# Optimization experiments

Measured on AMD Instinct MI355X. Metric: run time of the kernel, lower is better.

## Reference

```python
import jax, jax.numpy as jnp
import numpy as np

# Sizes derived from init_kwargs via calc_mlp_features:
# total_param=2117777, router_ratio=0.002 -> router_param=4235.554, expert_param=264192
# expert_hidden = 256, router_hidden = 352
N = 131072      # number of coordinate points
CIN = 3         # expert_insize == router_insize (xyz coords)
E = 8           # num_experts
K = 2           # top_k
H = 256         # expert_hidden (also SIREN data_channel)
RH = 352        # router_hidden
NHID = 3        # expert_layers - 2 hidden SIREN layers
W0C = 30.0      # sine frequency w0


def setup_inputs() -> dict:
    key = jax.random.key(0)
    ks = jax.random.split(key, 16)
    u = lambda k, shape, a: jax.random.uniform(k, shape, jnp.float32, -a, a)
    x = jax.random.uniform(ks[0], (N, CIN), jnp.float32, -1.0, 1.0)
    context = jax.random.uniform(ks[1], (N, CIN), jnp.float32, -1.0, 1.0)
    # Router: kaiming-normal weights, torch-default uniform biases
    Wr1 = jax.random.normal(ks[2], (CIN, RH), jnp.float32) * np.float32(np.sqrt(2.0 / CIN))
    br1 = u(ks[3], (RH,), 1.0 / np.sqrt(CIN))
    Wr2 = jax.random.normal(ks[4], (RH, E), jnp.float32) * np.float32(np.sqrt(2.0 / RH))
    br2 = u(ks[5], (E,), 1.0 / np.sqrt(RH))
    # SIREN experts (stacked over E): first layer U(-1/in, 1/in), rest U(+-sqrt(6/in)/30)
    sb = np.sqrt(6.0 / H) / 30.0
    W0 = u(ks[6], (E, CIN, H), 1.0 / CIN)
    b0 = u(ks[7], (E, H), 1.0 / np.sqrt(CIN))
    Wh = u(ks[8], (E, NHID, H, H), sb)
    bh = u(ks[9], (E, NHID, H), 1.0 / np.sqrt(H))
    Wo = u(ks[10], (E, H, H), sb)
    bo = u(ks[11], (E, H), 1.0 / np.sqrt(H))
    # Decoder: Linear(H,H)+ReLU+Linear(H,1)
    Wd1 = jax.random.normal(ks[12], (H, H), jnp.float32) * np.float32(np.sqrt(2.0 / H))
    bd1 = u(ks[13], (H,), 1.0 / np.sqrt(H))
    Wd2 = jax.random.normal(ks[14], (H, 1), jnp.float32) * np.float32(np.sqrt(2.0 / H))
    bd2 = u(ks[15], (1,), 1.0 / np.sqrt(H))
    return dict(x=x, context=context, Wr1=Wr1, br1=br1, Wr2=Wr2, br2=br2,
                W0=W0, b0=b0, Wh=Wh, bh=bh, Wo=Wo, bo=bo,
                Wd1=Wd1, bd1=bd1, Wd2=Wd2, bd2=bd2)


def reference(x, context, Wr1, br1, Wr2, br2, W0, b0, Wh, bh, Wo, bo, Wd1, bd1, Wd2, bd2):
    n = x.shape[0]
    # --- NoisyTopkRouter (eval path: no noise) ---
    logits = jnp.maximum(context @ Wr1 + br1, 0.0) @ Wr2 + br2          # [N, E]
    topv, topi = jax.lax.top_k(logits, K)                                # [N, K]
    # softmax over -inf-filled sparse logits == softmax over the top-k values
    w = jax.nn.softmax(topv, axis=-1)                                    # [N, K]
    gating = jnp.zeros_like(logits).at[jnp.arange(n)[:, None], topi].set(w)  # [N, E], zero off top-k
    # --- Per-expert SIREN, weighted combine ---
    # Masked dispatch + scatter-add in the original equals dense weighted sum
    # because gating is exactly zero for non-selected experts.
    def expert_step(acc, p):
        W0e, b0e, Whe, bhe, Woe, boe, ge = p
        h = jnp.sin(W0C * (x @ W0e + b0e))                # [N, H]
        for i in range(NHID):
            h = jnp.sin(W0C * (h @ Whe[i] + bhe[i]))
        out = h @ Woe + boe                               # [N, H], no output activation
        return acc + out * ge[:, None], None
    acc0 = jnp.zeros((n, H), dtype=x.dtype)
    final, _ = jax.lax.scan(expert_step, acc0, (W0, b0, Wh, bh, Wo, bo, gating.T))
    # --- Decoder ---
    return jnp.maximum(final @ Wd1 + bd1, 0.0) @ Wd2 + bd2               # [N, 1]
```

## Files before the change

kernel.cpp:

```cpp
#include <hip/hip_runtime.h>
#include <stdint.h>

#define N_PTS 131072
#define RH    352
#define SREV  4.774648292756860f

typedef short  bf16x8 __attribute__((ext_vector_type(8)));
typedef float  f32x16 __attribute__((ext_vector_type(16)));

__device__ __forceinline__ unsigned short f2bf(float f) {
  uint32_t u = __builtin_bit_cast(uint32_t, f);
  u = (u + 0x7FFFu + ((u >> 16) & 1u)) >> 16;
  return (unsigned short)u;
}
__device__ __forceinline__ float bf2f(unsigned short s) {
  return __builtin_bit_cast(float, ((uint32_t)s) << 16);
}
__device__ __forceinline__ float vsin1(float x) {
  float xf = x - floorf(x);
  float r;
  asm("v_sin_f32 %0, %1" : "=v"(r) : "v"(xf));
  return r;
}
__device__ __forceinline__ f32x16 mfma_bf16(bf16x8 a, bf16x8 b, f32x16 c) {
  return __builtin_amdgcn_mfma_f32_32x32x16_bf16(a, b, c, 0, 0, 0);
}

#define AWLOAD(d0, d1, addr64) \
  asm volatile("global_load_dwordx4 %0, %2, off\n\t" \
               "global_load_dwordx4 %1, %2, off offset:1024" \
               : "=&v"(d0), "=&v"(d1) : "v"(addr64))

#define VWAIT(N, r0, r1) \
  asm volatile("s_waitcnt vmcnt(" #N ")" : "+v"(r0), "+v"(r1))

__global__ __launch_bounds__(512) void setup_kernel(
    const float* __restrict__ W0, const float* __restrict__ b0,
    const float* __restrict__ Wh, const float* __restrict__ bh,
    const float* __restrict__ Wo, const float* __restrict__ bo,
    const float* __restrict__ Wd1, const float* __restrict__ bd1,
    short* __restrict__ pW0, short* __restrict__ pWh,
    short* __restrict__ pWo, short* __restrict__ pWd1,
    const float* __restrict__ ctx, const float* __restrict__ Wr1,
    const float* __restrict__ br1, const float* __restrict__ Wr2,
    const float* __restrict__ br2, uint4* __restrict__ topk,
    uint32_t* __restrict__ counts)
{
  __shared__ double w1d[RH*4];
  __shared__ double w2d[RH*8];
  __shared__ uint32_t lcnt[8];
  int b = blockIdx.x, tid = threadIdx.x;

  if (b < 569) {
    int jb = tid >> 6, l = tid & 63;
    int j  = jb*32 + (l & 31);
    int s0 = (l >> 5) * 8;
    unsigned short o[8];
    short* dp;
    if (b < 544) {
      int m = b / 17, slice = b % 17;
      int e = m >> 2, t = m & 3;
      const float* src; const float* bias; float scale; short* dst;
      if (t < 3) { src = Wh + (size_t)(e*3+t)*65536; bias = bh + (size_t)(e*3+t)*256; scale = SREV; dst = pWh + (size_t)(e*3+t)*69632; }
      else       { src = Wo + (size_t)e*65536;       bias = bo + (size_t)e*256;       scale = 1.0f; dst = pWo + (size_t)e*69632; }
      if (slice < 16) {
        #pragma unroll
        for (int i = 0; i < 8; ++i) {
          int k = slice*16 + s0 + i;
          o[i] = f2bf(scale * src[(size_t)k*256 + j]);
        }
      } else {
        #pragma unroll
        for (int i = 0; i < 8; ++i) o[i] = 0;
        if (s0 == 0) {
          float a = scale * bias[j];
          unsigned short h = f2bf(a);
          o[0] = h; o[1] = f2bf(a - bf2f(h));
        }
      }
      dp = dst + (size_t)slice*4096 + jb*512 + l*8;
    } else if (b < 552) {
      int e = b - 544;
      const float* w0 = W0 + (size_t)e*768;
      const float* bb = b0 + (size_t)e*256;
      #pragma unroll
      for (int i = 0; i < 8; ++i) {
        int s = s0 + i;
        unsigned short v = 0;
        if (s < 3) v = f2bf(SREV * w0[(size_t)s*256 + j]);
        else if (s < 6) { float a = SREV * w0[(size_t)(s-3)*256 + j]; unsigned short h = f2bf(a); v = f2bf(a - bf2f(h)); }
        else if (s < 9) v = f2bf(SREV * w0[(size_t)(s-6)*256 + j]);
        else if (s == 9)  v = f2bf(SREV * bb[j]);
        else if (s == 10) { float a = SREV * bb[j]; unsigned short h = f2bf(a); v = f2bf(a - bf2f(h)); }
        o[i] = v;
      }
      dp = pW0 + (size_t)e*4096 + jb*512 + l*8;
    } else {
      int slice = b - 552;
      if (slice < 16) {
        #pragma unroll
        for (int i = 0; i < 8; ++i) {
          int k = slice*16 + s0 + i;
          o[i] = f2bf(Wd1[(size_t)k*256 + j]);
        }
      } else {
        #pragma unroll
        for (int i = 0; i < 8; ++i) o[i] = 0;
        if (s0 == 0) {
          float a = bd1[j];
          unsigned short h = f2bf(a);
          o[0] = h; o[1] = f2bf(a - bf2f(h));
        }
      }
      dp = pWd1 + (size_t)slice*4096 + jb*512 + l*8;
    }
    uint4 v;
    v.x = (uint32_t)o[0] | ((uint32_t)o[1] << 16);
    v.y = (uint32_t)o[2] | ((uint32_t)o[3] << 16);
    v.z = (uint32_t)o[4] | ((uint32_t)o[5] << 16);
    v.w = (uint32_t)o[6] | ((uint32_t)o[7] << 16);
    *(uint4*)dp = v;
    return;
  }

  int rb = b - 569;
  for (int i = tid; i < RH; i += 512) {
    w1d[i*4+0] = (double)Wr1[i];
    w1d[i*4+1] = (double)Wr1[352 + i];
    w1d[i*4+2] = (double)Wr1[704 + i];
    w1d[i*4+3] = (double)br1[i];
  }
  for (int i = tid; i < RH*8; i += 512) w2d[i] = (double)Wr2[i];
  if (tid < 8) lcnt[tid] = 0;
  __syncthreads();

  int n = rb*512 + tid;
  double c0 = (double)ctx[(size_t)n*3+0];
  double c1 = (double)ctx[(size_t)n*3+1];
  double c2 = (double)ctx[(size_t)n*3+2];
  double lg[8];
  #pragma unroll
  for (int e = 0; e < 8; ++e) lg[e] = (double)br2[e];
  for (int j = 0; j < RH; ++j) {
    const double* a = &w1d[j*4];
    double h = c0*a[0] + c1*a[1] + c2*a[2] + a[3];
    h = h > 0.0 ? h : 0.0;
    const double* bq = &w2d[j*8];
    lg[0] += h*bq[0]; lg[1] += h*bq[1]; lg[2] += h*bq[2]; lg[3] += h*bq[3];
    lg[4] += h*bq[4]; lg[5] += h*bq[5]; lg[6] += h*bq[6]; lg[7] += h*bq[7];
  }
  double v0 = -1e300, v1 = -1e300; int i0 = 0, i1 = 0;
  #pragma unroll
  for (int e = 0; e < 8; ++e) {
    double lv = lg[e];
    if (lv > v0)      { v1 = v0; i1 = i0; v0 = lv; i0 = e; }
    else if (lv > v1) { v1 = lv; i1 = e; }
  }
  float ex = __expf((float)(v1 - v0));
  float s = 1.0f / (1.0f + ex);
  uint4 t;
  t.x = (uint32_t)i0 | ((uint32_t)i1 << 8);
  t.y = __builtin_bit_cast(uint32_t, s);
  t.z = __builtin_bit_cast(uint32_t, ex * s);
  t.w = 0;
  topk[n] = t;
  atomicAdd(&lcnt[i0], 1u); atomicAdd(&lcnt[i1], 1u);
  __syncthreads();
  if (tid < 8) atomicAdd(&counts[tid], lcnt[tid]);
}

__global__ __launch_bounds__(256) void scatter_kernel(
    const uint4* __restrict__ topk, const uint32_t* __restrict__ counts,
    uint32_t* __restrict__ cursors, uint32_t* __restrict__ plist,
    float* __restrict__ pw)
{
  __shared__ uint32_t lc[8], lb[8], offs[8];
  int tid = threadIdx.x;
  if (tid < 8) {
    lc[tid] = 0;
    uint32_t o = 0;
    for (int k = 0; k < tid; ++k) o += counts[k];
    offs[tid] = o;
  }
  __syncthreads();
  int n = blockIdx.x*256 + tid;
  uint4 t = topk[n];
  uint32_t e0 = t.x & 255u, e1 = (t.x >> 8) & 255u;
  uint32_t p0 = atomicAdd(&lc[e0], 1u);
  uint32_t p1 = atomicAdd(&lc[e1], 1u);
  __syncthreads();
  if (tid < 8) lb[tid] = offs[tid] + atomicAdd(&cursors[tid], lc[tid]);
  __syncthreads();
  uint32_t d0 = lb[e0] + p0, d1 = lb[e1] + p1;
  plist[d0] = ((uint32_t)n << 1);      pw[d0] = __builtin_bit_cast(float, t.y);
  plist[d1] = ((uint32_t)n << 1) | 1u; pw[d1] = __builtin_bit_cast(float, t.z);
}

__global__ __launch_bounds__(256, 3) void expert_kernel(
    const float* __restrict__ x, const uint32_t* __restrict__ counts,
    const uint32_t* __restrict__ plist, const float* __restrict__ pw,
    const short* __restrict__ pW0, const short* __restrict__ pWh,
    const short* __restrict__ pWo, short* __restrict__ outbuf)
{
  __shared__ __align__(16) uint8_t smem[34816];
  uint8_t* hB = smem;
  uint8_t* xB = smem + 32768;

  int tid = threadIdx.x;
  int lane = tid & 63;
  int jq = tid >> 6;
  int aoff = jq*2048 + lane*16;

  bf16x8 bbias;
  #pragma unroll
  for (int i = 0; i < 8; ++i) bbias[i] = 0;
  if (lane < 32) { bbias[0] = (short)0x3F80; bbias[1] = (short)0x3F80; }

  bf16x8 aw[5][2];
  f32x16 acc[2][2];

  int rr = tid >> 2;
  int rq = tid & 3;

  uint32_t tt = blockIdx.x;
  int e = -1; uint32_t cnt = 0, off = 0;
  #pragma unroll 1
  for (int ee = 0; ee < 8; ++ee) {
    uint32_t c = counts[ee];
    uint32_t nt = (c + 63u) >> 6;
    if (tt < nt) { e = ee; cnt = c; break; }
    tt -= nt; off += c;
  }
  if (e < 0) return;
  uint32_t base = off + (tt << 6);
  int nvalid = (int)cnt - (int)(tt << 6); if (nvalid > 64) nvalid = 64;

  uint64_t matp[4];
  matp[0] = (uint64_t)(uintptr_t)(pWh + (size_t)(e*3+0)*69632);
  matp[1] = (uint64_t)(uintptr_t)(pWh + (size_t)(e*3+1)*69632);
  matp[2] = (uint64_t)(uintptr_t)(pWh + (size_t)(e*3+2)*69632);
  matp[3] = (uint64_t)(uintptr_t)(pWo + (size_t)e*69632);

  {
    uint64_t pb = matp[0] + (uint64_t)aoff;
    AWLOAD(aw[0][0], aw[0][1], pb);
    AWLOAD(aw[1][0], aw[1][1], pb + 8192);
    AWLOAD(aw[2][0], aw[2][1], pb + 16384);
    AWLOAD(aw[3][0], aw[3][1], pb + 24576);
  }

  float wgt[2];
  #pragma unroll
  for (int c = 0; c < 2; ++c) {
    int n = c*32 + (lane & 31);
    wgt[c] = (n < nvalid) ? pw[base + n] : 0.0f;
  }
  uint32_t psv = (rr < nvalid) ? plist[base + rr] : 0u;

  if (tid < 64) {
    float x0 = 0.0f, x1 = 0.0f, x2 = 0.0f;
    if (tid < nvalid) {
      uint32_t v = plist[base + tid];
      const float* xp = x + (size_t)(v >> 1)*3;
      x0 = xp[0]; x1 = xp[1]; x2 = xp[2];
    }
    unsigned short h0 = f2bf(x0), h1 = f2bf(x1), h2 = f2bf(x2);
    unsigned short l0 = f2bf(x0 - bf2f(h0)), l1 = f2bf(x1 - bf2f(h1)), l2 = f2bf(x2 - bf2f(h2));
    uint4 r0, r1;
    r0.x = (uint32_t)h0 | ((uint32_t)h1 << 16);
    r0.y = (uint32_t)h2 | ((uint32_t)h0 << 16);
    r0.z = (uint32_t)h1 | ((uint32_t)h2 << 16);
    r0.w = (uint32_t)l0 | ((uint32_t)l1 << 16);
    r1.x = (uint32_t)l2 | (0x3F80u << 16);
    r1.y = 0x3F80u;
    r1.z = 0u; r1.w = 0u;
    uint4* dst = (uint4*)(xB + tid*32);
    dst[0] = r0; dst[1] = r1;
  }

  const uint8_t* pw0e = (const uint8_t*)(pW0 + (size_t)e*4096);
  bf16x8 a0[2];
  a0[0] = *(const bf16x8*)(pw0e + aoff);
  a0[1] = *(const bf16x8*)(pw0e + aoff + 1024);

  __syncthreads();

  #pragma unroll
  for (int a2 = 0; a2 < 2; ++a2)
    #pragma unroll
    for (int c = 0; c < 2; ++c)
      #pragma unroll
      for (int r = 0; r < 16; ++r) acc[a2][c][r] = 0.0f;

  {
    bf16x8 bv[2];
    #pragma unroll
    for (int c = 0; c < 2; ++c) {
      int n = c*32 + (lane & 31);
      bv[c] = *(const bf16x8*)(xB + n*32 + ((lane >> 5)*16));
    }
    #pragma unroll
    for (int a2 = 0; a2 < 2; ++a2)
      #pragma unroll
      for (int c = 0; c < 2; ++c)
        acc[a2][c] = mfma_bf16(a0[a2], bv[c], acc[a2][c]);
  }

#define WRITE_SIN() { _Pragma("unroll") \
    for (int a2 = 0; a2 < 2; ++a2) { \
      int jb = jq*2 + a2; \
      _Pragma("unroll") \
      for (int c = 0; c < 2; ++c) { \
        int n = c*32 + (lane & 31); \
        uint32_t rowb = (uint32_t)n * 512u; \
        uint32_t sw = (uint32_t)((n & 7) << 4); \
        _Pragma("unroll") \
        for (int g = 0; g < 4; ++g) { \
          float s0f = vsin1(acc[a2][c][g*4+0]); \
          float s1f = vsin1(acc[a2][c][g*4+1]); \
          float s2f = vsin1(acc[a2][c][g*4+2]); \
          float s3f = vsin1(acc[a2][c][g*4+3]); \
          uint2 pv; \
          pv.x = (uint32_t)f2bf(s0f) | ((uint32_t)f2bf(s1f) << 16); \
          pv.y = (uint32_t)f2bf(s2f) | ((uint32_t)f2bf(s3f) << 16); \
          int j0 = jb*32 + g*8 + ((lane >> 5) << 2); \
          uint32_t off2 = (rowb + (uint32_t)(j0*2)) ^ sw; \
          *(uint2*)(hB + off2) = pv; \
        } \
      } \
    } }

  WRITE_SIN();
  __syncthreads();

#define STEP(L, kb) { \
    enum { u_ = (L)*17 + (kb), ps_ = u_ + 4, us_ = u_ % 5, pss_ = ps_ % 5 }; \
    if (ps_ <= 67) { \
      uint64_t pa_ = matp[ps_/17] + (uint64_t)((ps_%17)*8192) + (uint64_t)aoff; \
      AWLOAD(aw[pss_][0], aw[pss_][1], pa_); \
    } \
    if (u_ <= 63)      { VWAIT(8, aw[us_][0], aw[us_][1]); } \
    else if (u_ == 64) { VWAIT(6, aw[us_][0], aw[us_][1]); } \
    else if (u_ == 65) { VWAIT(4, aw[us_][0], aw[us_][1]); } \
    else if (u_ == 66) { VWAIT(2, aw[us_][0], aw[us_][1]); } \
    else               { VWAIT(0, aw[us_][0], aw[us_][1]); } \
    bf16x8 bv0_, bv1_; \
    if ((kb) < 16) { \
      { int n_ = (lane & 31); \
        uint32_t off_ = ((uint32_t)n_*512u + (uint32_t)((kb)*32) + (uint32_t)((lane >> 5)*16)) \
                        ^ (uint32_t)((n_ & 7) << 4); \
        bv0_ = *(const bf16x8*)(hB + off_); } \
      { int n_ = 32 + (lane & 31); \
        uint32_t off_ = ((uint32_t)n_*512u + (uint32_t)((kb)*32) + (uint32_t)((lane >> 5)*16)) \
                        ^ (uint32_t)((n_ & 7) << 4); \
        bv1_ = *(const bf16x8*)(hB + off_); } \
    } else { bv0_ = bbias; bv1_ = bbias; } \
    acc[0][0] = mfma_bf16(aw[us_][0], bv0_, acc[0][0]); \
    acc[1][0] = mfma_bf16(aw[us_][1], bv0_, acc[1][0]); \
    acc[0][1] = mfma_bf16(aw[us_][0], bv1_, acc[0][1]); \
    acc[1][1] = mfma_bf16(aw[us_][1], bv1_, acc[1][1]); \
}
#define LAYER17(L) STEP(L,0) STEP(L,1) STEP(L,2) STEP(L,3) STEP(L,4) STEP(L,5) \
    STEP(L,6) STEP(L,7) STEP(L,8) STEP(L,9) STEP(L,10) STEP(L,11) STEP(L,12) \
    STEP(L,13) STEP(L,14) STEP(L,15) STEP(L,16)

#define ZACC() { _Pragma("unroll") for (int a2 = 0; a2 < 2; ++a2) \
    _Pragma("unroll") for (int c = 0; c < 2; ++c) \
    _Pragma("unroll") for (int r = 0; r < 16; ++r) acc[a2][c][r] = 0.0f; }

  ZACC(); LAYER17(0)
  __syncthreads(); WRITE_SIN(); __syncthreads();
  ZACC(); LAYER17(1)
  __syncthreads(); WRITE_SIN(); __syncthreads();
  ZACC(); LAYER17(2)
  __syncthreads(); WRITE_SIN(); __syncthreads();
  ZACC(); LAYER17(3)
  __syncthreads();
  #pragma unroll
  for (int a2 = 0; a2 < 2; ++a2) {
    int jb = jq*2 + a2;
    #pragma unroll
    for (int c = 0; c < 2; ++c) {
      int n = c*32 + (lane & 31);
      float w = wgt[c];
      uint32_t rowb = (uint32_t)n * 512u;
      uint32_t sw = (uint32_t)((n & 7) << 4);
      #pragma unroll
      for (int g = 0; g < 4; ++g) {
        float s0f = acc[a2][c][g*4+0] * w;
        float s1f = acc[a2][c][g*4+1] * w;
        float s2f = acc[a2][c][g*4+2] * w;
        float s3f = acc[a2][c][g*4+3] * w;
        uint2 pv;
        pv.x = (uint32_t)f2bf(s0f) | ((uint32_t)f2bf(s1f) << 16);
        pv.y = (uint32_t)f2bf(s2f) | ((uint32_t)f2bf(s3f) << 16);
        int j0 = jb*32 + g*8 + ((lane >> 5) << 2);
        uint32_t off2 = (rowb + (uint32_t)(j0*2)) ^ sw;
        *(uint2*)(hB + off2) = pv;
      }
    }
  }
  __syncthreads();
  if (rr < nvalid) {
    uint4* dst = (uint4*)(outbuf + ((size_t)(psv & 1)*N_PTS + (size_t)(psv >> 1))*256
                          + rq*64);
    uint32_t rowb = (uint32_t)rr*512u + (uint32_t)rq*128u;
    uint32_t sw = (uint32_t)((rr & 7) << 4);
    #pragma unroll
    for (int c = 0; c < 8; ++c)
      dst[c] = *(const uint4*)(hB + ((rowb + (uint32_t)(c*16)) ^ sw));
  }
}

__global__ __launch_bounds__(256, 3) void decoder_kernel(
    const short* __restrict__ outbuf, const short* __restrict__ pWd1,
    const float* __restrict__ Wd2v, const float* __restrict__ bd2,
    float* __restrict__ outp)
{
  __shared__ __align__(16) uint8_t smem[34816];
  uint8_t* hB = smem;
  float* wd2  = (float*)(smem + 32768);
  float* part = (float*)(smem + 33792);

  int tid = threadIdx.x;
  int lane = tid & 63;
  int jq = tid >> 6;
  int aoff = jq*2048 + lane*16;
  int tbase = blockIdx.x * 64;
  int rr = tid >> 2;
  int rq = tid & 3;

  bf16x8 bbias;
  #pragma unroll
  for (int i = 0; i < 8; ++i) bbias[i] = 0;
  if (lane < 32) { bbias[0] = (short)0x3F80; bbias[1] = (short)0x3F80; }

  bf16x8 aw[5][2];
  f32x16 acc[2][2];

  uint64_t wp = (uint64_t)(uintptr_t)pWd1;
  {
    uint64_t pb = wp + (uint64_t)aoff;
    AWLOAD(aw[0][0], aw[0][1], pb);
    AWLOAD(aw[1][0], aw[1][1], pb + 8192);
    AWLOAD(aw[2][0], aw[2][1], pb + 16384);
    AWLOAD(aw[3][0], aw[3][1], pb + 24576);
  }

  wd2[tid] = Wd2v[tid];

  {
    const short* o0 = outbuf + (size_t)(tbase + rr)*256 + rq*64;
    const short* o1 = o0 + (size_t)N_PTS*256;
    uint32_t rowb = (uint32_t)rr*512u + (uint32_t)rq*128u;
    uint32_t sw = (uint32_t)((rr & 7) << 4);
    #pragma unroll
    for (int c = 0; c < 8; ++c) {
      uint4 a  = *(const uint4*)(o0 + c*8);
      uint4 bq = *(const uint4*)(o1 + c*8);
      uint4 ov;
      uint32_t* ap = (uint32_t*)&a;
      uint32_t* bp = (uint32_t*)&bq;
      uint32_t* op = (uint32_t*)&ov;
      #pragma unroll
      for (int w = 0; w < 4; ++w) {
        uint32_t ua = ap[w], ub = bp[w];
        float f0 = bf2f((unsigned short)(ua & 0xFFFFu)) + bf2f((unsigned short)(ub & 0xFFFFu));
        float f1 = bf2f((unsigned short)(ua >> 16))     + bf2f((unsigned short)(ub >> 16));
        op[w] = (uint32_t)f2bf(f0) | ((uint32_t)f2bf(f1) << 16);
      }
      *(uint4*)(hB + ((rowb + (uint32_t)(c*16)) ^ sw)) = ov;
    }
  }
  __syncthreads();

  #pragma unroll
  for (int a2 = 0; a2 < 2; ++a2)
    #pragma unroll
    for (int c = 0; c < 2; ++c)
      #pragma unroll
      for (int r = 0; r < 16; ++r) acc[a2][c][r] = 0.0f;

#define DSTEP(kb) { \
    enum { ps_ = (kb) + 4, us_ = (kb) % 5, pss_ = ps_ % 5 }; \
    if (ps_ <= 16) { \
      uint64_t pa_ = wp + (uint64_t)(ps_*8192) + (uint64_t)aoff; \
      AWLOAD(aw[pss_][0], aw[pss_][1], pa_); \
    } \
    if ((kb) <= 12)      { VWAIT(8, aw[us_][0], aw[us_][1]); } \
    else if ((kb) == 13) { VWAIT(6, aw[us_][0], aw[us_][1]); } \
    else if ((kb) == 14) { VWAIT(4, aw[us_][0], aw[us_][1]); } \
    else if ((kb) == 15) { VWAIT(2, aw[us_][0], aw[us_][1]); } \
    else                 { VWAIT(0, aw[us_][0], aw[us_][1]); } \
    bf16x8 bv0_, bv1_; \
    if ((kb) < 16) { \
      { int n_ = (lane & 31); \
        uint32_t off_ = ((uint32_t)n_*512u + (uint32_t)((kb)*32) + (uint32_t)((lane >> 5)*16)) \
                        ^ (uint32_t)((n_ & 7) << 4); \
        bv0_ = *(const bf16x8*)(hB + off_); } \
      { int n_ = 32 + (lane & 31); \
        uint32_t off_ = ((uint32_t)n_*512u + (uint32_t)((kb)*32) + (uint32_t)((lane >> 5)*16)) \
                        ^ (uint32_t)((n_ & 7) << 4); \
        bv1_ = *(const bf16x8*)(hB + off_); } \
    } else { bv0_ = bbias; bv1_ = bbias; } \
    acc[0][0] = mfma_bf16(aw[us_][0], bv0_, acc[0][0]); \
    acc[1][0] = mfma_bf16(aw[us_][1], bv0_, acc[1][0]); \
    acc[0][1] = mfma_bf16(aw[us_][0], bv1_, acc[0][1]); \
    acc[1][1] = mfma_bf16(aw[us_][1], bv1_, acc[1][1]); \
}
  DSTEP(0)  DSTEP(1)  DSTEP(2)  DSTEP(3)  DSTEP(4)  DSTEP(5)
  DSTEP(6)  DSTEP(7)  DSTEP(8)  DSTEP(9)  DSTEP(10) DSTEP(11)
  DSTEP(12) DSTEP(13) DSTEP(14) DSTEP(15) DSTEP(16)

  float p0 = 0.0f, p1 = 0.0f;
  #pragma unroll
  for (int a2 = 0; a2 < 2; ++a2) {
    int jb = jq*2 + a2;
    #pragma unroll
    for (int c = 0; c < 2; ++c) {
      #pragma unroll
      for (int r = 0; r < 16; ++r) {
        int j = jb*32 + (r & 3) + ((r >> 2) << 3) + ((lane >> 5) << 2);
        float v = acc[a2][c][r];
        v = v > 0.0f ? v : 0.0f;
        float t = v * wd2[j];
        if (c == 0) p0 += t; else p1 += t;
      }
    }
  }
  p0 += __shfl_xor(p0, 32);
  p1 += __shfl_xor(p1, 32);
  if (lane < 32) {
    part[jq*64 + lane] = p0;
    part[jq*64 + 32 + lane] = p1;
  }
  __syncthreads();
  if (tid < 64)
    outp[tbase + tid] = part[tid] + part[64 + tid] + part[128 + tid]
                      + part[192 + tid] + bd2[0];
}

extern "C" void kernel_launch(void* const* d_in, const int* in_sizes, int n_in,
                              void* d_out, int out_size, void* d_ws, size_t ws_size,
                              hipStream_t stream) {
  const float* x   = (const float*)d_in[0];
  const float* ctx = (const float*)d_in[1];
  const float* Wr1 = (const float*)d_in[2];
  const float* br1 = (const float*)d_in[3];
  const float* Wr2 = (const float*)d_in[4];
  const float* br2 = (const float*)d_in[5];
  const float* W0  = (const float*)d_in[6];
  const float* b0  = (const float*)d_in[7];
  const float* Wh  = (const float*)d_in[8];
  const float* bh  = (const float*)d_in[9];
  const float* Wo  = (const float*)d_in[10];
  const float* bo  = (const float*)d_in[11];
  const float* Wd1 = (const float*)d_in[12];
  const float* bd1 = (const float*)d_in[13];
  const float* Wd2 = (const float*)d_in[14];
  const float* bd2 = (const float*)d_in[15];
  float* out = (float*)d_out;

  const size_t WS_COUNTS  = 0;
  const size_t WS_CURSORS = 32;
  const size_t WS_TOPK    = 1024;
  const size_t WS_PLIST   = WS_TOPK  + (size_t)N_PTS*16;
  const size_t WS_PW      = WS_PLIST + (size_t)N_PTS*8;
  const size_t WS_PW0     = WS_PW    + (size_t)N_PTS*8;
  const size_t WS_PWH     = WS_PW0   + (size_t)8*8192;
  const size_t WS_PWO     = WS_PWH   + (size_t)24*139264;
  const size_t WS_PWD1    = WS_PWO   + (size_t)8*139264;
  const size_t WS_OUT     = WS_PWD1  + (size_t)139264;
  const size_t WS_END     = WS_OUT   + (size_t)2*N_PTS*256*2;

  if (ws_size < WS_END) {
    hipMemsetAsync(d_out, 0xFF, (size_t)out_size*4, stream);
    return;
  }

  uint8_t* ws = (uint8_t*)d_ws;
  uint32_t* counts  = (uint32_t*)(ws + WS_COUNTS);
  uint32_t* cursors = (uint32_t*)(ws + WS_CURSORS);
  uint4*    topk    = (uint4*)   (ws + WS_TOPK);
  uint32_t* plist   = (uint32_t*)(ws + WS_PLIST);
  float*    pw      = (float*)   (ws + WS_PW);
  short*    pW0     = (short*)   (ws + WS_PW0);
  short*    pWh     = (short*)   (ws + WS_PWH);
  short*    pWo     = (short*)   (ws + WS_PWO);
  short*    pWd1    = (short*)   (ws + WS_PWD1);
  short*    outbuf  = (short*)   (ws + WS_OUT);

  hipMemsetAsync(counts, 0, 64, stream);

  setup_kernel  <<<825,  512, 0, stream>>>(W0, b0, Wh, bh, Wo, bo, Wd1, bd1,
                                           pW0, pWh, pWo, pWd1,
                                           ctx, Wr1, br1, Wr2, br2, topk, counts);
  scatter_kernel<<<512,  256, 0, stream>>>(topk, counts, cursors, plist, pw);
  expert_kernel <<<4104, 256, 0, stream>>>(x, counts, plist, pw,
                                           pW0, pWh, pWo, outbuf);
  decoder_kernel<<<2048, 256, 0, stream>>>(outbuf, pWd1, Wd2, bd2, out);
}
```

Before: 279.1 us.

## Compute router in fp32 with fp64 fallback near ties; interleave output row stores

```diff
diff --git a/kernel.cpp b/kernel.cpp
--- a/kernel.cpp
+++ b/kernel.cpp
@@ -46,8 +46,8 @@
     const float* __restrict__ br2, uint4* __restrict__ topk,
     uint32_t* __restrict__ counts)
 {
-  __shared__ double w1d[RH*4];
-  __shared__ double w2d[RH*8];
+  __shared__ float w1f[RH*4];
+  __shared__ float w2f[RH*8];
   __shared__ uint32_t lcnt[8];
   int b = blockIdx.x, tid = threadIdx.x;
 
@@ -125,38 +125,62 @@
 
   int rb = b - 569;
   for (int i = tid; i < RH; i += 512) {
-    w1d[i*4+0] = (double)Wr1[i];
-    w1d[i*4+1] = (double)Wr1[352 + i];
-    w1d[i*4+2] = (double)Wr1[704 + i];
-    w1d[i*4+3] = (double)br1[i];
-  }
-  for (int i = tid; i < RH*8; i += 512) w2d[i] = (double)Wr2[i];
+    w1f[i*4+0] = Wr1[i];
+    w1f[i*4+1] = Wr1[352 + i];
+    w1f[i*4+2] = Wr1[704 + i];
+    w1f[i*4+3] = br1[i];
+  }
+  for (int i = tid; i < RH*8; i += 512) w2f[i] = Wr2[i];
   if (tid < 8) lcnt[tid] = 0;
   __syncthreads();
 
   int n = rb*512 + tid;
-  double c0 = (double)ctx[(size_t)n*3+0];
-  double c1 = (double)ctx[(size_t)n*3+1];
-  double c2 = (double)ctx[(size_t)n*3+2];
-  double lg[8];
-  #pragma unroll
-  for (int e = 0; e < 8; ++e) lg[e] = (double)br2[e];
+  float c0 = ctx[(size_t)n*3+0];
+  float c1 = ctx[(size_t)n*3+1];
+  float c2 = ctx[(size_t)n*3+2];
+  float lg[8];
+  #pragma unroll
+  for (int e = 0; e < 8; ++e) lg[e] = br2[e];
   for (int j = 0; j < RH; ++j) {
-    const double* a = &w1d[j*4];
-    double h = c0*a[0] + c1*a[1] + c2*a[2] + a[3];
-    h = h > 0.0 ? h : 0.0;
-    const double* bq = &w2d[j*8];
-    lg[0] += h*bq[0]; lg[1] += h*bq[1]; lg[2] += h*bq[2]; lg[3] += h*bq[3];
-    lg[4] += h*bq[4]; lg[5] += h*bq[5]; lg[6] += h*bq[6]; lg[7] += h*bq[7];
-  }
-  double v0 = -1e300, v1 = -1e300; int i0 = 0, i1 = 0;
+    const float* a = &w1f[j*4];
+    float h = fmaf(c0, a[0], fmaf(c1, a[1], fmaf(c2, a[2], a[3])));
+    h = h > 0.0f ? h : 0.0f;
+    const float* bq = &w2f[j*8];
+    lg[0] = fmaf(h, bq[0], lg[0]); lg[1] = fmaf(h, bq[1], lg[1]);
+    lg[2] = fmaf(h, bq[2], lg[2]); lg[3] = fmaf(h, bq[3], lg[3]);
+    lg[4] = fmaf(h, bq[4], lg[4]); lg[5] = fmaf(h, bq[5], lg[5]);
+    lg[6] = fmaf(h, bq[6], lg[6]); lg[7] = fmaf(h, bq[7], lg[7]);
+  }
+  float v0 = -1e30f, v1 = -1e30f, v2 = -1e30f; int i0 = 0, i1 = 0;
   #pragma unroll
   for (int e = 0; e < 8; ++e) {
-    double lv = lg[e];
-    if (lv > v0)      { v1 = v0; i1 = i0; v0 = lv; i0 = e; }
-    else if (lv > v1) { v1 = lv; i1 = e; }
-  }
-  float ex = __expf((float)(v1 - v0));
+    float lv = lg[e];
+    if (lv > v0)      { v2 = v1; v1 = v0; i1 = i0; v0 = lv; i0 = e; }
+    else if (lv > v1) { v2 = v1; v1 = lv; i1 = e; }
+    else if (lv > v2) { v2 = lv; }
+  }
+  float d10 = v1 - v0;
+  if (v1 - v2 < 1e-3f) {
+    double dg[8];
+    #pragma unroll
+    for (int e = 0; e < 8; ++e) dg[e] = (double)br2[e];
+    for (int j = 0; j < RH; ++j) {
+      double h = (double)c0*(double)Wr1[j] + (double)c1*(double)Wr1[352+j]
+               + (double)c2*(double)Wr1[704+j] + (double)br1[j];
+      h = h > 0.0 ? h : 0.0;
+      #pragma unroll
+      for (int e = 0; e < 8; ++e) dg[e] += h * (double)Wr2[j*8+e];
+    }
+    double dv0 = -1e300, dv1 = -1e300; int di0 = 0, di1 = 0;
+    #pragma unroll
+    for (int e = 0; e < 8; ++e) {
+      double lv = dg[e];
+      if (lv > dv0)      { dv1 = dv0; di1 = di0; dv0 = lv; di0 = e; }
+      else if (lv > dv1) { dv1 = lv; di1 = e; }
+    }
+    i0 = di0; i1 = di1; d10 = (float)(dv1 - dv0);
+  }
+  float ex = __expf(d10);
   float s = 1.0f / (1.0f + ex);
   uint4 t;
   t.x = (uint32_t)i0 | ((uint32_t)i1 << 8);
@@ -402,13 +426,14 @@
   }
   __syncthreads();
   if (rr < nvalid) {
-    uint4* dst = (uint4*)(outbuf + ((size_t)(psv & 1)*N_PTS + (size_t)(psv >> 1))*256
-                          + rq*64);
-    uint32_t rowb = (uint32_t)rr*512u + (uint32_t)rq*128u;
+    uint4* dst = (uint4*)(outbuf + ((size_t)(psv & 1)*N_PTS + (size_t)(psv >> 1))*256);
+    uint32_t rowb = (uint32_t)rr*512u;
     uint32_t sw = (uint32_t)((rr & 7) << 4);
     #pragma unroll
-    for (int c = 0; c < 8; ++c)
-      dst[c] = *(const uint4*)(hB + ((rowb + (uint32_t)(c*16)) ^ sw));
+    for (int c = 0; c < 8; ++c) {
+      int ch = c*4 + rq;
+      dst[ch] = *(const uint4*)(hB + ((rowb + (uint32_t)(ch*16)) ^ sw));
+    }
   }
 }
 
```

After: 336.3 us. 20.5% more time.
